# Kernel tuning notes

Measured on AMD Instinct MI355X. Metric: run time of the kernel, lower is better.

## Reference

```python
import jax, jax.numpy as jnp
import numpy as np

EPS = 1e-6


def setup_inputs() -> dict:
    key = jax.random.key(0)
    k1, k2, k3, k4, k5, k6, k7 = jax.random.split(key, 7)
    B, S, D, P = 16384, 8, 128, 65536
    return {
        "z_samples": jax.random.normal(k1, (B, S, D), dtype=jnp.float32),
        "alpha": jax.random.normal(k2, (), dtype=jnp.float32),
        "beta": jax.random.normal(k3, (), dtype=jnp.float32),
        "ap": jax.random.randint(k4, (P,), 0, B),
        "p": jax.random.randint(k5, (P,), 0, B),
        "an": jax.random.randint(k6, (P,), 0, B),
        "n": jax.random.randint(k7, (P,), 0, B),
    }


def _pairwise_sqdist(Xa, Xb):
    # Xa, Xb: [P, S, D] -> d2: [P, S, S] where d2[p,i,j] = ||Xa[p,i]-Xb[p,j]||^2
    S = Xa.shape[1]
    rows = []
    for i in range(S):  # S is a small fixed constant (n_samples)
        diff = Xa[:, i, None, :] - Xb  # [P, S, D]
        rows.append(jnp.sum(diff * diff, axis=-1))  # [P, S]
    return jnp.stack(rows, axis=1)  # [P, S, S]


def reference(z_samples, alpha, beta, ap, p, an, n):
    S = z_samples.shape[1]
    a = jax.nn.softplus(alpha)
    d2_pos = _pairwise_sqdist(z_samples[ap], z_samples[p])  # [P, S, S]
    d2_neg = _pairwise_sqdist(z_samples[an], z_samples[n])  # [P, S, S]
    prob_pos = jax.nn.sigmoid(-a * d2_pos + beta) + EPS
    prob_neg = jax.nn.sigmoid(-a * d2_neg + beta) + EPS
    per_pair = jnp.sum(-jnp.log(prob_pos) - jnp.log(1.0 - prob_neg), axis=(1, 2))
    per_pair = per_pair / (S * S)
    return jnp.mean(per_pair)
```

## Files before the change

kernel.cpp:

```cpp
#include <hip/hip_runtime.h>


typedef __attribute__((ext_vector_type(8))) short bf16x8;
typedef __attribute__((ext_vector_type(4))) float f32x4;
typedef __attribute__((ext_vector_type(8))) int v8i;

#define EPS 1e-6f
#define BLOCK_THREADS 256
#define WAVES_PER_BLOCK (BLOCK_THREADS / 64)
#define NPAIR 8
#define DEPTH 4

__device__ __forceinline__ unsigned fp4_of(float x) {
    float ax = __builtin_fabsf(x);
    unsigned m = (unsigned)(ax >= 0.25f) + (unsigned)(ax >= 0.75f)
               + (unsigned)(ax >= 1.25f) + (unsigned)(ax >= 1.75f)
               + (unsigned)(ax >= 2.5f)  + (unsigned)(ax >= 3.5f)
               + (unsigned)(ax >= 5.0f);
    return m | ((__builtin_bit_cast(unsigned, x) >> 28) & 8u);
}

__global__ __launch_bounds__(BLOCK_THREADS) void prep_kernel(
    const float* __restrict__ z,
    unsigned* __restrict__ zq32,
    float* __restrict__ norms,
    float* __restrict__ out0,
    int totalChunks, int strideChunks)
{
    if (blockIdx.x == 0 && threadIdx.x == 0) *out0 = 0.0f;

    const int lane = threadIdx.x & 63;
    const int wv   = threadIdx.x >> 6;
    const int wave = blockIdx.x * WAVES_PER_BLOCK + wv;
    const int rg   = lane >> 4;
    const int part = lane & 15;

    for (int chunk = wave; chunk < totalChunks; chunk += strideChunks) {
        const size_t rowIdx = (size_t)chunk * 4 + rg;
        const size_t off = rowIdx * 128 + (size_t)part * 8;
        const float4* src = (const float4*)(z + off);
        float4 c0 = src[0], c1 = src[1];

        float nrm = 0.0f;
        nrm = fmaf(c0.x, c0.x, nrm); nrm = fmaf(c0.y, c0.y, nrm);
        nrm = fmaf(c0.z, c0.z, nrm); nrm = fmaf(c0.w, c0.w, nrm);
        nrm = fmaf(c1.x, c1.x, nrm); nrm = fmaf(c1.y, c1.y, nrm);
        nrm = fmaf(c1.z, c1.z, nrm); nrm = fmaf(c1.w, c1.w, nrm);

        unsigned pk = fp4_of(c0.x)        | (fp4_of(c0.y) << 4)
                    | (fp4_of(c0.z) << 8) | (fp4_of(c0.w) << 12)
                    | (fp4_of(c1.x) << 16)| (fp4_of(c1.y) << 20)
                    | (fp4_of(c1.z) << 24)| (fp4_of(c1.w) << 28);
        zq32[rowIdx * 16 + part] = pk;

        nrm += __shfl_xor(nrm, 1, 64);
        nrm += __shfl_xor(nrm, 2, 64);
        nrm += __shfl_xor(nrm, 4, 64);
        nrm += __shfl_xor(nrm, 8, 64);
        if (part == 0) norms[rowIdx] = nrm;
    }
}

__device__ __forceinline__ void issue_loads_fp4(
    const unsigned char* __restrict__ zq, const float* __restrict__ norms,
    int ia, int ib, int rr, int q,
    uint4& fa, uint4& fb, float& na, float& nb)
{
    fa = *(const uint4*)(zq + (size_t)ia * 512 + rr * 64 + q * 16);
    fb = *(const uint4*)(zq + (size_t)ib * 512 + rr * 64 + q * 16);
    na = norms[ia * 8 + rr];
    nb = norms[ib * 8 + rr];
}

__device__ __forceinline__ float pair_epilogue_fp4(
    const uint4& fau, const uint4& fbu, float na, float nb,
    float a, float negb, int q, float sgn, float eps_sgn, float one_p,
    float valid_f)
{
    v8i a8, b8;
    a8[0] = fau.x; a8[1] = fau.y; a8[2] = fau.z; a8[3] = fau.w;
    a8[4] = fau.x; a8[5] = fau.y; a8[6] = fau.z; a8[7] = fau.w;
    b8[0] = fbu.x; b8[1] = fbu.y; b8[2] = fbu.z; b8[3] = fbu.w;
    b8[4] = fbu.x; b8[5] = fbu.y; b8[6] = fbu.z; b8[7] = fbu.w;

    f32x4 acc = {0.f, 0.f, 0.f, 0.f};
    acc = __builtin_amdgcn_mfma_scale_f32_16x16x128_f8f6f4(
        a8, b8, acc, 4, 4, 0, 0x7F, 0, 0x7F);

    float den = 1.0f, num = 1.0f;
    #pragma unroll
    for (int reg = 0; reg < 4; ++reg) {
        const int row = q * 4 + reg;
        const float nArow = __shfl(na, row, 64);
        const float ssum = nArow + nb;
        const float d2 = fmaf(-2.0f, acc[reg], ssum);
        const float u = fmaf(a, d2, negb);
        float x = u * sgn;
        x = fminf(x, 20.0f);
        const float E = __expf(x);
        den *= (1.0f + E);
        num *= fmaf(eps_sgn, E, one_p);
    }
    const float pl = __log2f(den) - __log2f(num);
    return valid_f * pl;
}

__global__ __launch_bounds__(BLOCK_THREADS) void hib_main(
    const unsigned char* __restrict__ zq,
    const float* __restrict__ norms,
    const float* __restrict__ alpha,
    const float* __restrict__ beta,
    const int* __restrict__ ap,
    const int* __restrict__ pp,
    const int* __restrict__ an,
    const int* __restrict__ nn,
    float* __restrict__ out,
    int P, float scale)
{
    __shared__ float red[WAVES_PER_BLOCK];

    const int lane  = threadIdx.x & 63;
    const int wv    = threadIdx.x >> 6;
    const int gwave = blockIdx.x * WAVES_PER_BLOCK + wv;
    const int pairBase = __builtin_amdgcn_readfirstlane(gwave * NPAIR);

    const float a    = log1pf(expf(alpha[0]));
    const float negb = -beta[0];

    const int r  = lane & 15;
    const int q  = lane >> 4;
    const int rr = r & 7;
    const bool topA = (r < 8);
    const bool pos_side = (q < 2);
    const float valid_f = (pos_side == topA) ? 1.0f : 0.0f;
    const float sgn     = pos_side ? 1.0f : -1.0f;
    const float eps_sgn = pos_side ? EPS : -EPS;
    const float one_p   = 1.0f + eps_sgn;

    float loss = 0.0f;

    if (pairBase + NPAIR <= P) {
        const int4 A0 = *(const int4*)(ap + pairBase);
        const int4 A1 = *(const int4*)(ap + pairBase + 4);
        const int4 P0 = *(const int4*)(pp + pairBase);
        const int4 P1 = *(const int4*)(pp + pairBase + 4);
        const int4 N0 = *(const int4*)(an + pairBase);
        const int4 N1 = *(const int4*)(an + pairBase + 4);
        const int4 M0 = *(const int4*)(nn + pairBase);
        const int4 M1 = *(const int4*)(nn + pairBase + 4);
        const int iap[NPAIR] = {A0.x, A0.y, A0.z, A0.w, A1.x, A1.y, A1.z, A1.w};
        const int ipp[NPAIR] = {P0.x, P0.y, P0.z, P0.w, P1.x, P1.y, P1.z, P1.w};
        const int ian[NPAIR] = {N0.x, N0.y, N0.z, N0.w, N1.x, N1.y, N1.z, N1.w};
        const int inn[NPAIR] = {M0.x, M0.y, M0.z, M0.w, M1.x, M1.y, M1.z, M1.w};

        uint4 fa[DEPTH], fb[DEPTH];
        float na[DEPTH], nb[DEPTH];

        #pragma unroll
        for (int k = 0; k < DEPTH - 1; ++k) {
            issue_loads_fp4(zq, norms,
                            topA ? iap[k] : ian[k], topA ? ipp[k] : inn[k],
                            rr, q, fa[k], fb[k], na[k], nb[k]);
        }

        #pragma unroll
        for (int k = 0; k < NPAIR; ++k) {
            const int cur = k & (DEPTH - 1);
            if (k + DEPTH - 1 < NPAIR) {
                const int nxt = (k + DEPTH - 1) & (DEPTH - 1);
                issue_loads_fp4(zq, norms,
                                topA ? iap[k + DEPTH - 1] : ian[k + DEPTH - 1],
                                topA ? ipp[k + DEPTH - 1] : inn[k + DEPTH - 1],
                                rr, q, fa[nxt], fb[nxt], na[nxt], nb[nxt]);
            }
            loss += pair_epilogue_fp4(fa[cur], fb[cur], na[cur], nb[cur],
                                      a, negb, q, sgn, eps_sgn, one_p, valid_f);
        }
    } else if (pairBase < P) {
        for (int k = 0; k < NPAIR; ++k) {
            const int pr = pairBase + k;
            if (pr >= P) break;
            const int ia = topA ? ap[pr] : an[pr];
            const int ib = topA ? pp[pr] : nn[pr];
            uint4 tfa, tfb; float tna, tnb;
            issue_loads_fp4(zq, norms, ia, ib, rr, q, tfa, tfb, tna, tnb);
            loss += pair_epilogue_fp4(tfa, tfb, tna, tnb,
                                      a, negb, q, sgn, eps_sgn, one_p, valid_f);
        }
    }

    #pragma unroll
    for (int off = 32; off > 0; off >>= 1)
        loss += __shfl_down(loss, off, 64);
    if (lane == 0) red[wv] = loss;
    __syncthreads();
    if (threadIdx.x == 0) {
        float s = 0.0f;
        #pragma unroll
        for (int w = 0; w < WAVES_PER_BLOCK; ++w) s += red[w];
        atomicAdd(out, s * scale);
    }
}

__device__ __forceinline__ unsigned pack2_bf16(float lo, float hi) {
    unsigned ulo = __builtin_bit_cast(unsigned, lo) + 0x8000u;
    unsigned uhi = __builtin_bit_cast(unsigned, hi) + 0x8000u;
    return __builtin_amdgcn_perm(uhi, ulo, 0x07060302);
}

union FragAB { bf16x8 v; unsigned u[4]; };

__device__ __forceinline__ void fill_frag(FragAB& f, float4 c0, float4 c1, float& norm) {
    f.u[0] = pack2_bf16(c0.x, c0.y);
    f.u[1] = pack2_bf16(c0.z, c0.w);
    f.u[2] = pack2_bf16(c1.x, c1.y);
    f.u[3] = pack2_bf16(c1.z, c1.w);
    norm = fmaf(c0.x, c0.x, norm); norm = fmaf(c0.y, c0.y, norm);
    norm = fmaf(c0.z, c0.z, norm); norm = fmaf(c0.w, c0.w, norm);
    norm = fmaf(c1.x, c1.x, norm); norm = fmaf(c1.y, c1.y, norm);
    norm = fmaf(c1.z, c1.z, norm); norm = fmaf(c1.w, c1.w, norm);
}

__global__ __launch_bounds__(BLOCK_THREADS) void hib_fallback(
    const float* __restrict__ z,
    const float* __restrict__ alpha,
    const float* __restrict__ beta,
    const int* __restrict__ ap,
    const int* __restrict__ pp_idx,
    const int* __restrict__ an,
    const int* __restrict__ nn_idx,
    float* __restrict__ out,
    int P, int totalWaves, float scale)
{
    __shared__ float red[WAVES_PER_BLOCK];
    const int lane  = threadIdx.x & 63;
    const int wv    = threadIdx.x >> 6;
    const int gwave = blockIdx.x * WAVES_PER_BLOCK + wv;
    const float a = log1pf(expf(alpha[0]));
    const float b = beta[0];
    const int r = lane & 15;
    const int q = lane >> 4;
    const int rr = r & 7;
    const bool pos_side = (q < 2);
    const bool valid = (pos_side == (r < 8));
    const float eps_sgn = pos_side ? EPS : -EPS;
    float loss = 0.0f;

    if (gwave == 0 && lane == 0 && wv == 0) {}

    for (int pair = gwave; pair < P; pair += totalWaves) {
        const int idxA = (r < 8) ? ap[pair] : an[pair];
        const int idxB = (r < 8) ? pp_idx[pair] : nn_idx[pair];
        const float* rowA = z + (size_t)idxA * 1024 + rr * 128 + q * 8;
        const float* rowB = z + (size_t)idxB * 1024 + rr * 128 + q * 8;
        f32x4 acc = {0.f, 0.f, 0.f, 0.f};
        float na = 0.f, nb = 0.f;
        #pragma unroll
        for (int kb = 0; kb < 4; ++kb) {
            const float4* pa = (const float4*)(rowA + kb * 32);
            const float4* pb = (const float4*)(rowB + kb * 32);
            float4 a0 = pa[0], a1 = pa[1];
            float4 b0 = pb[0], b1 = pb[1];
            FragAB fav, fbv;
            fill_frag(fav, a0, a1, na);
            fill_frag(fbv, b0, b1, nb);
            acc = __builtin_amdgcn_mfma_f32_16x16x32_bf16(fav.v, fbv.v, acc, 0, 0, 0);
        }
        na += __shfl_xor(na, 16, 64);
        na += __shfl_xor(na, 32, 64);
        nb += __shfl_xor(nb, 16, 64);
        nb += __shfl_xor(nb, 32, 64);
        float cell = 0.0f;
        #pragma unroll
        for (int reg = 0; reg < 4; ++reg) {
            const int row = q * 4 + reg;
            const float nArow = __shfl(na, row, 64);
            const float d2 = nArow + nb - 2.0f * acc[reg];
            float t = fmaf(-a, d2, b);
            const float t_adj = pos_side ? -t : t;
            const float s = 1.0f / (1.0f + __expf(t_adj)) + eps_sgn;
            cell += -__logf(s);
        }
        if (valid) loss += cell;
    }

    #pragma unroll
    for (int off = 32; off > 0; off >>= 1)
        loss += __shfl_down(loss, off, 64);
    if (lane == 0) red[wv] = loss;
    __syncthreads();
    if (threadIdx.x == 0) {
        float s = 0.0f;
        #pragma unroll
        for (int w = 0; w < WAVES_PER_BLOCK; ++w) s += red[w];
        atomicAdd(out, s * scale);
    }
}

extern "C" void kernel_launch(void* const* d_in, const int* in_sizes, int n_in,
                              void* d_out, int out_size, void* d_ws, size_t ws_size,
                              hipStream_t stream) {
    const float* z     = (const float*)d_in[0];
    const float* alpha = (const float*)d_in[1];
    const float* beta  = (const float*)d_in[2];
    const int*   ap    = (const int*)d_in[3];
    const int*   p     = (const int*)d_in[4];
    const int*   an    = (const int*)d_in[5];
    const int*   n     = (const int*)d_in[6];
    float* out = (float*)d_out;

    const int P = in_sizes[3];
    const int zElems = in_sizes[0];
    const int totalRows = zElems / 128;

    const size_t zqBytes = (size_t)totalRows * 64;
    const size_t need = zqBytes + (size_t)totalRows * sizeof(float);

    if (ws_size >= need) {
        unsigned char* zq = (unsigned char*)d_ws;
        float* norms = (float*)((char*)d_ws + zqBytes);

        const int totalChunks = totalRows / 4;
        const int prepBlocks = 2048;
        prep_kernel<<<prepBlocks, BLOCK_THREADS, 0, stream>>>(
            z, (unsigned*)zq, norms, out, totalChunks, prepBlocks * WAVES_PER_BLOCK);

        const int totalWaves = (P + NPAIR - 1) / NPAIR;
        const int blocks = (totalWaves + WAVES_PER_BLOCK - 1) / WAVES_PER_BLOCK;
        const float scale = 0.6931471805599453f / ((float)P * 64.0f);

        hib_main<<<blocks, BLOCK_THREADS, 0, stream>>>(
            zq, norms, alpha, beta, ap, p, an, n, out, P, scale);
    } else {
        hipMemsetAsync(out, 0, sizeof(float), stream);
        const int blocks = 4096;
        const int totalWaves = blocks * WAVES_PER_BLOCK;
        const float scale = 1.0f / ((float)P * 64.0f);
        hib_fallback<<<blocks, BLOCK_THREADS, 0, stream>>>(
            z, alpha, beta, ap, p, an, n, out, P, totalWaves, scale);
    }
    (void)n_in; (void)out_size;
}
```

Before: 136.2 us.

## Compute row norms via extra FP4 MFMAs instead of storing fp32 norms

Drops the fp32 norm computation and storage from the prep kernel and the per-pair norm gathers in the main kernel. Norms are instead taken from the diagonals of two extra MFMA self-products (A·A and B·B) on the quantized fragments and moved into place with shuffles. All eight pairs' loads are now issued up front rather than through a depth-4 rotating buffer, and the main kernel gains an occupancy hint in its launch bounds. This cuts memory traffic and norm-load latency at the cost of three MFMAs per pair instead of one. Norms now come from quantized values, which changes numerics but keeps them consistent with the quantized dot product.

```diff
diff --git a/kernel.cpp b/kernel.cpp
--- a/kernel.cpp
+++ b/kernel.cpp
@@ -9,7 +9,6 @@
 #define BLOCK_THREADS 256
 #define WAVES_PER_BLOCK (BLOCK_THREADS / 64)
 #define NPAIR 8
-#define DEPTH 4
 
 __device__ __forceinline__ unsigned fp4_of(float x) {
     float ax = __builtin_fabsf(x);
@@ -23,7 +22,6 @@
 __global__ __launch_bounds__(BLOCK_THREADS) void prep_kernel(
     const float* __restrict__ z,
     unsigned* __restrict__ zq32,
-    float* __restrict__ norms,
     float* __restrict__ out0,
     int totalChunks, int strideChunks)
 {
@@ -41,40 +39,26 @@
         const float4* src = (const float4*)(z + off);
         float4 c0 = src[0], c1 = src[1];
 
-        float nrm = 0.0f;
-        nrm = fmaf(c0.x, c0.x, nrm); nrm = fmaf(c0.y, c0.y, nrm);
-        nrm = fmaf(c0.z, c0.z, nrm); nrm = fmaf(c0.w, c0.w, nrm);
-        nrm = fmaf(c1.x, c1.x, nrm); nrm = fmaf(c1.y, c1.y, nrm);
-        nrm = fmaf(c1.z, c1.z, nrm); nrm = fmaf(c1.w, c1.w, nrm);
-
         unsigned pk = fp4_of(c0.x)        | (fp4_of(c0.y) << 4)
                     | (fp4_of(c0.z) << 8) | (fp4_of(c0.w) << 12)
                     | (fp4_of(c1.x) << 16)| (fp4_of(c1.y) << 20)
                     | (fp4_of(c1.z) << 24)| (fp4_of(c1.w) << 28);
         zq32[rowIdx * 16 + part] = pk;
-
-        nrm += __shfl_xor(nrm, 1, 64);
-        nrm += __shfl_xor(nrm, 2, 64);
-        nrm += __shfl_xor(nrm, 4, 64);
-        nrm += __shfl_xor(nrm, 8, 64);
-        if (part == 0) norms[rowIdx] = nrm;
     }
 }
 
 __device__ __forceinline__ void issue_loads_fp4(
-    const unsigned char* __restrict__ zq, const float* __restrict__ norms,
+    const unsigned char* __restrict__ zq,
     int ia, int ib, int rr, int q,
-    uint4& fa, uint4& fb, float& na, float& nb)
+    uint4& fa, uint4& fb)
 {
     fa = *(const uint4*)(zq + (size_t)ia * 512 + rr * 64 + q * 16);
     fb = *(const uint4*)(zq + (size_t)ib * 512 + rr * 64 + q * 16);
-    na = norms[ia * 8 + rr];
-    nb = norms[ib * 8 + rr];
 }
 
 __device__ __forceinline__ float pair_epilogue_fp4(
-    const uint4& fau, const uint4& fbu, float na, float nb,
-    float a, float negb, int q, float sgn, float eps_sgn, float one_p,
+    const uint4& fau, const uint4& fbu,
+    float a, float negb, int r, int q, float sgn, float eps_sgn, float one_p,
     float valid_f)
 {
     v8i a8, b8;
@@ -83,17 +67,32 @@
     b8[0] = fbu.x; b8[1] = fbu.y; b8[2] = fbu.z; b8[3] = fbu.w;
     b8[4] = fbu.x; b8[5] = fbu.y; b8[6] = fbu.z; b8[7] = fbu.w;
 
-    f32x4 acc = {0.f, 0.f, 0.f, 0.f};
-    acc = __builtin_amdgcn_mfma_scale_f32_16x16x128_f8f6f4(
-        a8, b8, acc, 4, 4, 0, 0x7F, 0, 0x7F);
+    f32x4 accG = {0.f, 0.f, 0.f, 0.f};
+    f32x4 accA = {0.f, 0.f, 0.f, 0.f};
+    f32x4 accB = {0.f, 0.f, 0.f, 0.f};
+    accG = __builtin_amdgcn_mfma_scale_f32_16x16x128_f8f6f4(
+        a8, b8, accG, 4, 4, 0, 0x7F, 0, 0x7F);
+    accA = __builtin_amdgcn_mfma_scale_f32_16x16x128_f8f6f4(
+        a8, a8, accA, 4, 4, 0, 0x7F, 0, 0x7F);
+    accB = __builtin_amdgcn_mfma_scale_f32_16x16x128_f8f6f4(
+        b8, b8, accB, 4, 4, 0, 0x7F, 0, 0x7F);
+
+    const int sub = r & 3;
+    float tA0 = (sub & 1) ? accA[1] : accA[0];
+    float tA1 = (sub & 1) ? accA[3] : accA[2];
+    float dA  = (sub & 2) ? tA1 : tA0;
+    float tB0 = (sub & 1) ? accB[1] : accB[0];
+    float tB1 = (sub & 1) ? accB[3] : accB[2];
+    float dB  = (sub & 2) ? tB1 : tB0;
+
+    const float nb = __shfl(dB, r + ((r >> 2) << 4), 64);
 
     float den = 1.0f, num = 1.0f;
     #pragma unroll
     for (int reg = 0; reg < 4; ++reg) {
         const int row = q * 4 + reg;
-        const float nArow = __shfl(na, row, 64);
-        const float ssum = nArow + nb;
-        const float d2 = fmaf(-2.0f, acc[reg], ssum);
+        const float nArow = __shfl(dA, row + ((row >> 2) << 4), 64);
+        const float d2 = fmaf(-2.0f, accG[reg], nArow + nb);
         const float u = fmaf(a, d2, negb);
         float x = u * sgn;
         x = fminf(x, 20.0f);
@@ -105,9 +104,8 @@
     return valid_f * pl;
 }
 
-__global__ __launch_bounds__(BLOCK_THREADS) void hib_main(
+__global__ __launch_bounds__(BLOCK_THREADS, 4) void hib_main(
     const unsigned char* __restrict__ zq,
-    const float* __restrict__ norms,
     const float* __restrict__ alpha,
     const float* __restrict__ beta,
     const int* __restrict__ ap,
@@ -153,28 +151,17 @@
         const int ian[NPAIR] = {N0.x, N0.y, N0.z, N0.w, N1.x, N1.y, N1.z, N1.w};
         const int inn[NPAIR] = {M0.x, M0.y, M0.z, M0.w, M1.x, M1.y, M1.z, M1.w};
 
-        uint4 fa[DEPTH], fb[DEPTH];
-        float na[DEPTH], nb[DEPTH];
-
-        #pragma unroll
-        for (int k = 0; k < DEPTH - 1; ++k) {
-            issue_loads_fp4(zq, norms,
+        uint4 fa[NPAIR], fb[NPAIR];
+        #pragma unroll
+        for (int k = 0; k < NPAIR; ++k) {
+            issue_loads_fp4(zq,
                             topA ? iap[k] : ian[k], topA ? ipp[k] : inn[k],
-                            rr, q, fa[k], fb[k], na[k], nb[k]);
-        }
-
+                            rr, q, fa[k], fb[k]);
+        }
         #pragma unroll
         for (int k = 0; k < NPAIR; ++k) {
-            const int cur = k & (DEPTH - 1);
-            if (k + DEPTH - 1 < NPAIR) {
-                const int nxt = (k + DEPTH - 1) & (DEPTH - 1);
-                issue_loads_fp4(zq, norms,
-                                topA ? iap[k + DEPTH - 1] : ian[k + DEPTH - 1],
-                                topA ? ipp[k + DEPTH - 1] : inn[k + DEPTH - 1],
-                                rr, q, fa[nxt], fb[nxt], na[nxt], nb[nxt]);
-            }
-            loss += pair_epilogue_fp4(fa[cur], fb[cur], na[cur], nb[cur],
-                                      a, negb, q, sgn, eps_sgn, one_p, valid_f);
+            loss += pair_epilogue_fp4(fa[k], fb[k],
+                                      a, negb, r, q, sgn, eps_sgn, one_p, valid_f);
         }
     } else if (pairBase < P) {
         for (int k = 0; k < NPAIR; ++k) {
@@ -182,10 +169,10 @@
             if (pr >= P) break;
             const int ia = topA ? ap[pr] : an[pr];
             const int ib = topA ? pp[pr] : nn[pr];
-            uint4 tfa, tfb; float tna, tnb;
-            issue_loads_fp4(zq, norms, ia, ib, rr, q, tfa, tfb, tna, tnb);
-            loss += pair_epilogue_fp4(tfa, tfb, tna, tnb,
-                                      a, negb, q, sgn, eps_sgn, one_p, valid_f);
+            uint4 tfa, tfb;
+            issue_loads_fp4(zq, ia, ib, rr, q, tfa, tfb);
+            loss += pair_epilogue_fp4(tfa, tfb,
+                                      a, negb, r, q, sgn, eps_sgn, one_p, valid_f);
         }
     }
 
@@ -246,8 +233,6 @@
     const float eps_sgn = pos_side ? EPS : -EPS;
     float loss = 0.0f;
 
-    if (gwave == 0 && lane == 0 && wv == 0) {}
-
     for (int pair = gwave; pair < P; pair += totalWaves) {
         const int idxA = (r < 8) ? ap[pair] : an[pair];
         const int idxB = (r < 8) ? pp_idx[pair] : nn_idx[pair];
@@ -313,24 +298,22 @@
     const int zElems = in_sizes[0];
     const int totalRows = zElems / 128;
 
-    const size_t zqBytes = (size_t)totalRows * 64;
-    const size_t need = zqBytes + (size_t)totalRows * sizeof(float);
+    const size_t need = (size_t)totalRows * 64;
 
     if (ws_size >= need) {
         unsigned char* zq = (unsigned char*)d_ws;
-        float* norms = (float*)((char*)d_ws + zqBytes);
 
         const int totalChunks = totalRows / 4;
         const int prepBlocks = 2048;
         prep_kernel<<<prepBlocks, BLOCK_THREADS, 0, stream>>>(
-            z, (unsigned*)zq, norms, out, totalChunks, prepBlocks * WAVES_PER_BLOCK);
+            z, (unsigned*)zq, out, totalChunks, prepBlocks * WAVES_PER_BLOCK);
 
         const int totalWaves = (P + NPAIR - 1) / NPAIR;
         const int blocks = (totalWaves + WAVES_PER_BLOCK - 1) / WAVES_PER_BLOCK;
         const float scale = 0.6931471805599453f / ((float)P * 64.0f);
 
         hib_main<<<blocks, BLOCK_THREADS, 0, stream>>>(
-            zq, norms, alpha, beta, ap, p, an, n, out, P, scale);
+            zq, alpha, beta, ap, p, an, n, out, P, scale);
     } else {
         hipMemsetAsync(out, 0, sizeof(float), stream);
         const int blocks = 4096;
```

Result: no change. 137.4 us (+0.9%).
